# Kernel tuning notes

Hardware: AMD Instinct MI355X
Metric: run time of the kernel (lower is better)

The kernel has to match this reference:

```python
import jax, jax.numpy as jnp
import numpy as np

NUM_HEADS = 16
ROPE_BASE = 2048.0


def _rope_tables(seq_len, head_dim, dtype):
    inv_freq = 1.0 / (ROPE_BASE ** (jnp.arange(0, head_dim, 2, dtype=jnp.float32) / head_dim))
    t = jnp.arange(seq_len, dtype=jnp.float32)
    freqs = jnp.einsum('i,j->ij', t, inv_freq)          # [N, D/2]
    emb = jnp.concatenate([freqs, freqs], axis=-1)       # [N, D]
    return jnp.cos(emb).astype(dtype), jnp.sin(emb).astype(dtype)


def _rotate_half(x):
    x1, x2 = jnp.split(x, 2, axis=-1)
    return jnp.concatenate([-x2, x1], axis=-1)


def setup_inputs() -> dict:
    key = jax.random.key(0)
    k1, k2, k3, k4 = jax.random.split(key, 4)
    B, N, C = 2, 2048, 1024
    x = jax.random.normal(k1, (B, N, C), dtype=jnp.float32)
    w_qkv = jax.random.normal(k2, (3 * C, C), dtype=jnp.float32) * (C ** -0.5)
    w_proj = jax.random.normal(k3, (C, C), dtype=jnp.float32) * (C ** -0.5)
    b_proj = jnp.zeros((C,), dtype=jnp.float32)
    key_padding_mask = jax.random.randint(k4, (B, N), 0, 2, dtype=jnp.int32)
    return {"x": x, "w_qkv": w_qkv, "w_proj": w_proj, "b_proj": b_proj,
            "key_padding_mask": key_padding_mask}


def reference(x, w_qkv, w_proj, b_proj, key_padding_mask):
    B, N, C = x.shape
    H = NUM_HEADS
    D = C // H
    scale = D ** -0.5

    qkv = x @ w_qkv.T                                    # [B, N, 3C]
    q, k, v = jnp.split(qkv, 3, axis=-1)
    # [B, N, C] -> [B, H, N, D]
    q = q.reshape(B, N, H, D).transpose(0, 2, 1, 3)
    k = k.reshape(B, N, H, D).transpose(0, 2, 1, 3)
    v = v.reshape(B, N, H, D).transpose(0, 2, 1, 3)

    cos, sin = _rope_tables(N, D, x.dtype)               # [N, D]
    q = q * cos + _rotate_half(q) * sin
    k = k * cos + _rotate_half(k) * sin

    attn = jnp.einsum('bhqd,bhkd->bhqk', q, k) * scale   # [B, H, N, N]
    mask = (key_padding_mask == 0)[:, None, None, :]     # [B, 1, 1, N]
    attn = jnp.where(mask, jnp.asarray(-1e9, attn.dtype), attn)
    attn = jax.nn.softmax(attn, axis=-1)

    out = jnp.einsum('bhqk,bhkd->bhqd', attn, v)         # [B, H, N, D]
    out = out.transpose(0, 2, 1, 3).reshape(B, N, C)
    return out @ w_proj.T + b_proj
```

## Files before the change

### kernel.cpp

```cpp
#include <hip/hip_runtime.h>


typedef __attribute__((ext_vector_type(8))) short          s16x8;
typedef __attribute__((ext_vector_type(8))) unsigned short u16x8;
typedef __attribute__((ext_vector_type(4))) unsigned short u16x4;
typedef __attribute__((ext_vector_type(4))) float          f32x4;
typedef __attribute__((ext_vector_type(16))) float         f32x16;
typedef __attribute__((ext_vector_type(4))) unsigned int   u32x4;

#define MFMA_BF16(a, b, c) __builtin_amdgcn_mfma_f32_16x16x32_bf16((a), (b), (c), 0, 0, 0)
#define MFMA32_BF16(a, b, c) __builtin_amdgcn_mfma_f32_32x32x16_bf16((a), (b), (c), 0, 0, 0)

#define GLD_TO_LDS(gp, lp) __builtin_amdgcn_global_load_lds(                  \
    (const __attribute__((address_space(1))) void*)(gp),                      \
    (__attribute__((address_space(3))) void*)(lp), 16, 0, 0)

__device__ __forceinline__ unsigned short f2bf(float f) {
    union { float f; unsigned int u; } v; v.f = f;
    unsigned int u = v.u;
    unsigned int r = u + 0x7FFFu + ((u >> 16) & 1u);
    return (unsigned short)(r >> 16);
}
__device__ __forceinline__ float bf2f(unsigned short h) {
    union { unsigned int u; float f; } v; v.u = ((unsigned int)h) << 16;
    return v.f;
}
__device__ __forceinline__ f32x16 zero16() {
    f32x16 z;
#pragma unroll
    for (int i = 0; i < 16; i++) z[i] = 0.f;
    return z;
}
__device__ __forceinline__ unsigned int pkbf(float a, float b) {
    return __builtin_amdgcn_perm(__builtin_bit_cast(unsigned int, b),
                                 __builtin_bit_cast(unsigned int, a), 0x07060302u);
}
__device__ __forceinline__ int perm16(int p) {
    return (p & 3) + 8 * ((p >> 2) & 1) + 4 * (p >> 3);
}

__global__ __launch_bounds__(256) void prep(const float* __restrict__ x,
                                            const float* __restrict__ wqkv,
                                            const float* __restrict__ wproj,
                                            const int* __restrict__ m,
                                            unsigned short* __restrict__ xb,
                                            unsigned short* __restrict__ wqkvb,
                                            unsigned short* __restrict__ wprojb,
                                            unsigned short* __restrict__ mb) {
    int blk = blockIdx.x, tid = threadIdx.x;
    if (blk < 8192) {
        const float* src; unsigned short* dst; int i;
        if (blk < 4096)      { src = x;     dst = xb;     i = blk * 256 + tid; }
        else if (blk < 7168) { src = wqkv;  dst = wqkvb;  i = (blk - 4096) * 256 + tid; }
        else                 { src = wproj; dst = wprojb; i = (blk - 7168) * 256 + tid; }
        f32x4 v = ((const f32x4*)src)[i];
        u16x4 o;
        o[0] = f2bf(v[0]); o[1] = f2bf(v[1]); o[2] = f2bf(v[2]); o[3] = f2bf(v[3]);
        ((u16x4*)dst)[i] = o;
    } else {
        int i = (blk - 8192) * 256 + tid;
        int src = (i & ~15) | perm16(i & 15);
        mb[i] = (m[src] == 0) ? (unsigned short)0 : (unsigned short)0x3F80;
    }
}

__global__ __launch_bounds__(256) void gemm_bt(const unsigned short* __restrict__ A,
                                               const unsigned short* __restrict__ B,
                                               unsigned short* __restrict__ C,
                                               int M, int N, int K) {
    __shared__ unsigned short Al[128][64];
    __shared__ unsigned short Bl[128][64];
    const int tid  = threadIdx.x;
    const int lane = tid & 63;
    const int qd   = lane >> 4;
    const int cc   = lane & 15;
    const int wave = tid >> 6;
    const int wr   = wave >> 1, wc = wave & 1;
    const int nbx  = N >> 7;
    const int nwg  = gridDim.x;
    int d = blockIdx.x;
    int s = (nwg % 8 == 0) ? (d % 8) * (nwg / 8) + d / 8 : d;
    const int m0   = (s / nbx) * 128, n0 = (s % nbx) * 128;
    unsigned short* Alf = &Al[0][0];
    unsigned short* Blf = &Bl[0][0];

    f32x4 acc[4][4];
#pragma unroll
    for (int i = 0; i < 4; i++)
#pragma unroll
        for (int j = 0; j < 4; j++) acc[i][j] = (f32x4){0.f, 0.f, 0.f, 0.f};

    for (int k0 = 0; k0 < K; k0 += 64) {
#pragma unroll
        for (int t = 0; t < 4; t++) {
            int idx = t * 256 + tid;
            int row = idx >> 3, sg = (idx & 7) ^ (row & 7);
            GLD_TO_LDS(A + (size_t)(m0 + row) * K + k0 + sg * 8, Alf + idx * 8);
            GLD_TO_LDS(B + (size_t)(n0 + row) * K + k0 + sg * 8, Blf + idx * 8);
        }
        __syncthreads();
#pragma unroll
        for (int ks = 0; ks < 64; ks += 32) {
            const int s4 = ks >> 3;
            s16x8 af[4], bf[4];
#pragma unroll
            for (int i = 0; i < 4; i++) {
                int r = wr * 64 + i * 16 + cc;
                af[i] = *(const s16x8*)&Al[r][((s4 + qd) ^ (r & 7)) * 8];
            }
#pragma unroll
            for (int j = 0; j < 4; j++) {
                int r = wc * 64 + j * 16 + cc;
                bf[j] = *(const s16x8*)&Bl[r][((s4 + qd) ^ (r & 7)) * 8];
            }
#pragma unroll
            for (int i = 0; i < 4; i++)
#pragma unroll
                for (int j = 0; j < 4; j++)
                    acc[i][j] = MFMA_BF16(af[i], bf[j], acc[i][j]);
        }
        __syncthreads();
    }
#pragma unroll
    for (int i = 0; i < 4; i++)
#pragma unroll
        for (int j = 0; j < 4; j++)
#pragma unroll
            for (int r = 0; r < 4; r++) {
                int row = m0 + wr * 64 + i * 16 + qd * 4 + r;
                int col = n0 + wc * 64 + j * 16 + cc;
                C[(size_t)row * N + col] = f2bf(acc[i][j][r]);
            }
}

__global__ __launch_bounds__(256) void rope_scatter(const unsigned short* __restrict__ qkv,
                                                    const int* __restrict__ msk,
                                                    unsigned short* __restrict__ Q,
                                                    unsigned short* __restrict__ Kg,
                                                    unsigned short* __restrict__ Vt) {
    const int N = 2048, H = 16, D = 64, C3 = 3072;
    const float SCL = 0.18033688f;
    __shared__ unsigned short vl[64][65];
    const int nt = blockIdx.x, h = blockIdx.y, b = blockIdx.z;
    const int n0 = nt * 64;
    const int tid = threadIdx.x;
    const size_t bh = (size_t)b * H + h;
#pragma unroll
    for (int it = 0; it < 2; it++) {
        int idx = tid + it * 256;
        int row = idx >> 3, seg = idx & 7;
        int d0 = seg * 8;
        int n = n0 + row;
        size_t rb = ((size_t)b * N + n) * C3;
        int keep = msk[(size_t)b * N + n];
        u16x8 qv = *(const u16x8*)&qkv[rb + h * 64 + d0];
        u16x8 qp = *(const u16x8*)&qkv[rb + h * 64 + (d0 ^ 32)];
        u16x8 kv = *(const u16x8*)&qkv[rb + 1024 + h * 64 + d0];
        u16x8 kp = *(const u16x8*)&qkv[rb + 1024 + h * 64 + (d0 ^ 32)];
        u16x8 vv = *(const u16x8*)&qkv[rb + 2048 + h * 64 + d0];
        u16x8 qo, ko;
        float sgn = (d0 < 32) ? -1.0f : 1.0f;
#pragma unroll
        for (int j = 0; j < 8; j++) {
            int jj = (d0 & 31) + j;
            float th = (float)n * exp2f(-0.34375f * (float)jj);
            float cth = cosf(th), sth = sinf(th);
            qo[j] = f2bf((bf2f(qv[j]) * cth + sgn * bf2f(qp[j]) * sth) * SCL);
            ko[j] = f2bf(bf2f(kv[j]) * cth + sgn * bf2f(kp[j]) * sth);
            vl[row][d0 + j] = keep ? vv[j] : (unsigned short)0;
        }
        *(u16x8*)&Q[(bh * N + n) * D + d0]  = qo;
        *(u16x8*)&Kg[(bh * N + n) * D + d0] = ko;
    }
    __syncthreads();
#pragma unroll
    for (int it = 0; it < 2; it++) {
        int idx = tid + it * 256;
        int drow = idx >> 3, nseg = idx & 7;
        u16x8 ov;
#pragma unroll
        for (int j = 0; j < 8; j++) {
            int cpos = nseg * 8 + j;
            int srcl = (cpos & ~15) | perm16(cpos & 15);
            ov[j] = vl[srcl][drow];
        }
        *(u16x8*)&Vt[(bh * D + drow) * N + n0 + nseg * 8] = ov;
    }
}

__global__ __launch_bounds__(256, 2) void flash_attn(const unsigned short* __restrict__ Q,
                                                     const unsigned short* __restrict__ Kg,
                                                     const unsigned short* __restrict__ Vt,
                                                     const unsigned short* __restrict__ mb,
                                                     unsigned short* __restrict__ Og) {
    const int N = 2048, H = 16, D = 64;
    __shared__ unsigned short Kl0[64][64], Kl1[64][64];
    __shared__ unsigned short Vl0[64][64], Vl1[64][64];
    const int tid  = threadIdx.x;
    const int lane = tid & 63;
    const int wave = tid >> 6;
    const int c    = lane & 31;
    const int hi   = lane >> 5;
    int dd = blockIdx.x;
    int sw = (dd & 7) * 64 + (dd >> 3);
    const int qt = sw & 15, h = (sw >> 4) & 15, b = sw >> 8;
    const int q0 = qt * 128;
    const size_t bh = (size_t)b * H + h;

    s16x8 qf[4];
    {
        const unsigned short* Qb = Q + (bh * N + q0 + wave * 32 + c) * D;
#pragma unroll
        for (int kd = 0; kd < 4; kd++) qf[kd] = *(const s16x8*)(Qb + kd * 16 + hi * 8);
    }

    f32x16 o[2], lacc;
    o[0] = zero16(); o[1] = zero16(); lacc = zero16();

    const unsigned short* Kbase = Kg + bh * N * D;
    const unsigned short* Vbase = Vt + bh * D * N;
    const unsigned short* mbase = mb + (size_t)b * N;
    const int row_s = tid >> 3, sg_s = (tid & 7) ^ ((tid >> 3) & 7);
    const int row_s2 = (tid + 256) >> 3, sg_s2 = (tid & 7) ^ (((tid + 256) >> 3) & 7);

    auto issue = [&](int k0, unsigned short* Kb, unsigned short* Vb) {
        GLD_TO_LDS(Kbase + (size_t)(k0 + row_s) * D + sg_s * 8,   Kb + tid * 8);
        GLD_TO_LDS(Vbase + (size_t)row_s * N + k0 + sg_s * 8,     Vb + tid * 8);
        GLD_TO_LDS(Kbase + (size_t)(k0 + row_s2) * D + sg_s2 * 8, Kb + (tid + 256) * 8);
        GLD_TO_LDS(Vbase + (size_t)row_s2 * N + k0 + sg_s2 * 8,   Vb + (tid + 256) * 8);
    };

    auto compute = [&](int k0, const unsigned short (*Kb)[64], const unsigned short (*Vb)[64]) {
        f32x16 sst[2];
        __builtin_amdgcn_s_setprio(1);
#pragma unroll
        for (int kg = 0; kg < 2; kg++) {
            int kr = kg * 32 + c;
            f32x16 s = zero16();
#pragma unroll
            for (int kd = 0; kd < 4; kd++) {
                s16x8 kf = *(const s16x8*)&Kb[kr][((kd * 2 + hi) ^ (kr & 7)) * 8];
                s = MFMA32_BF16(kf, qf[kd], s);
            }
            sst[kg] = s;
        }
        __builtin_amdgcn_s_setprio(0);

        auto packkg = [&](int kg, s16x8* pa) {
            float p[16];
#pragma unroll
            for (int r = 0; r < 16; r++) p[r] = __builtin_amdgcn_exp2f(sst[kg][r]);
#pragma unroll
            for (int half = 0; half < 2; half++) {
                int bs = half * 8;
                u32x4 w = { pkbf(p[bs + 0], p[bs + 1]), pkbf(p[bs + 2], p[bs + 3]),
                            pkbf(p[bs + 4], p[bs + 5]), pkbf(p[bs + 6], p[bs + 7]) };
                pa[half] = __builtin_bit_cast(s16x8, w);
            }
        };

        auto pvks = [&](int ks, s16x8 pf) {
            s16x8 mfr = *(const s16x8*)&mbase[k0 + ks * 16 + hi * 8];
            __builtin_amdgcn_s_setprio(1);
            lacc = MFMA32_BF16(pf, mfr, lacc);
#pragma unroll
            for (int db = 0; db < 2; db++) {
                int vr = db * 32 + c;
                s16x8 vf = *(const s16x8*)&Vb[vr][((ks * 2 + hi) ^ (vr & 7)) * 8];
                o[db] = MFMA32_BF16(pf, vf, o[db]);
            }
            __builtin_amdgcn_s_setprio(0);
        };

        s16x8 pa[2];
        packkg(0, pa);
        pvks(0, pa[0]);
        pvks(1, pa[1]);
        packkg(1, pa);
        pvks(2, pa[0]);
        pvks(3, pa[1]);
    };

    issue(0, &Kl0[0][0], &Vl0[0][0]);
    __syncthreads();
    for (int it = 0; it < 32; it += 2) {
        int k0 = it * 64;
        if (it + 1 < 32) issue(k0 + 64, &Kl1[0][0], &Vl1[0][0]);
        compute(k0, Kl0, Vl0);
        __syncthreads();
        if (it + 2 < 32) issue(k0 + 128, &Kl0[0][0], &Vl0[0][0]);
        compute(k0 + 64, Kl1, Vl1);
        __syncthreads();
    }

    float linv[16];
#pragma unroll
    for (int r = 0; r < 16; r++) linv[r] = 1.0f / lacc[r];
#pragma unroll
    for (int db = 0; db < 2; db++)
#pragma unroll
        for (int r = 0; r < 16; r++) {
            int n = q0 + wave * 32 + (r & 3) + 8 * (r >> 2) + 4 * hi;
            Og[((size_t)b * N + n) * 1024 + h * 64 + db * 32 + c] =
                f2bf(o[db][r] * linv[r]);
        }
}

__global__ __launch_bounds__(256) void gemm_proj(const unsigned short* __restrict__ A,
                                                 const unsigned short* __restrict__ B,
                                                 float* __restrict__ C,
                                                 const float* __restrict__ bias) {
    const int NN = 1024, K = 1024;
    __shared__ unsigned short Al[128][64];
    __shared__ unsigned short Bl[64][64];
    const int tid  = threadIdx.x;
    const int lane = tid & 63;
    const int qd   = lane >> 4;
    const int cc   = lane & 15;
    const int wave = tid >> 6;
    const int wr   = wave >> 1, wc = wave & 1;
    int dd = blockIdx.x;
    int sw = (dd & 7) * 64 + (dd >> 3);
    const int m0   = (sw >> 4) * 128, n0 = (sw & 15) * 64;
    unsigned short* Alf = &Al[0][0];
    unsigned short* Blf = &Bl[0][0];

    f32x4 acc[4][2];
#pragma unroll
    for (int i = 0; i < 4; i++)
#pragma unroll
        for (int j = 0; j < 2; j++) acc[i][j] = (f32x4){0.f, 0.f, 0.f, 0.f};

    for (int k0 = 0; k0 < K; k0 += 64) {
#pragma unroll
        for (int t = 0; t < 4; t++) {
            int idx = t * 256 + tid;
            int row = idx >> 3, sg = (idx & 7) ^ (row & 7);
            GLD_TO_LDS(A + (size_t)(m0 + row) * K + k0 + sg * 8, Alf + idx * 8);
        }
#pragma unroll
        for (int t = 0; t < 2; t++) {
            int idx = t * 256 + tid;
            int row = idx >> 3, sg = (idx & 7) ^ (row & 7);
            GLD_TO_LDS(B + (size_t)(n0 + row) * K + k0 + sg * 8, Blf + idx * 8);
        }
        __syncthreads();
#pragma unroll
        for (int ks = 0; ks < 64; ks += 32) {
            const int s4 = ks >> 3;
            s16x8 af[4], bf[2];
#pragma unroll
            for (int i = 0; i < 4; i++) {
                int r = wr * 64 + i * 16 + cc;
                af[i] = *(const s16x8*)&Al[r][((s4 + qd) ^ (r & 7)) * 8];
            }
#pragma unroll
            for (int j = 0; j < 2; j++) {
                int r = wc * 32 + j * 16 + cc;
                bf[j] = *(const s16x8*)&Bl[r][((s4 + qd) ^ (r & 7)) * 8];
            }
#pragma unroll
            for (int i = 0; i < 4; i++)
#pragma unroll
                for (int j = 0; j < 2; j++)
                    acc[i][j] = MFMA_BF16(af[i], bf[j], acc[i][j]);
        }
        __syncthreads();
    }
#pragma unroll
    for (int i = 0; i < 4; i++)
#pragma unroll
        for (int j = 0; j < 2; j++)
#pragma unroll
            for (int r = 0; r < 4; r++) {
                int row = m0 + wr * 64 + i * 16 + qd * 4 + r;
                int col = n0 + wc * 32 + j * 16 + cc;
                C[(size_t)row * NN + col] = acc[i][j][r] + bias[col];
            }
}

extern "C" void kernel_launch(void* const* d_in, const int* in_sizes, int n_in,
                              void* d_out, int out_size, void* d_ws, size_t ws_size,
                              hipStream_t stream) {
    const float* x      = (const float*)d_in[0];
    const float* w_qkv  = (const float*)d_in[1];
    const float* w_proj = (const float*)d_in[2];
    const float* b_proj = (const float*)d_in[3];
    const int*   mask   = (const int*)d_in[4];
    float* out = (float*)d_out;

    unsigned short* ws     = (unsigned short*)d_ws;
    unsigned short* xb     = ws;
    unsigned short* wqkvb  = xb     + (size_t)4096 * 1024;
    unsigned short* wprojb = wqkvb  + (size_t)3072 * 1024;
    unsigned short* qkv    = wprojb + (size_t)1024 * 1024;
    unsigned short* Qm     = qkv    + (size_t)4096 * 3072;
    unsigned short* Km     = Qm     + (size_t)32 * 2048 * 64;
    unsigned short* Vtm    = Km     + (size_t)32 * 2048 * 64;
    unsigned short* attno  = Vtm    + (size_t)32 * 2048 * 64;
    unsigned short* maskbf = attno  + (size_t)4096 * 1024;

    prep<<<8208, 256, 0, stream>>>(x, w_qkv, w_proj, mask, xb, wqkvb, wprojb, maskbf);
    gemm_bt<<<768, 256, 0, stream>>>(xb, wqkvb, qkv, 4096, 3072, 1024);
    rope_scatter<<<dim3(32, 16, 2), 256, 0, stream>>>(qkv, mask, Qm, Km, Vtm);
    flash_attn<<<512, 256, 0, stream>>>(Qm, Km, Vtm, maskbf, attno);
    gemm_proj<<<512, 256, 0, stream>>>(attno, wprojb, out, b_proj);
}
```

Before: 185.8 us.

## Load K/V fragments directly from global into registers, dropping LDS staging

The flash attention kernel stops staging K and V tiles in shared memory through global_load_lds double buffering. Each wave now loads its K, V and mask fragments straight from global memory into registers, double-buffering K in registers, and all __syncthreads barriers are removed. This removes LDS traffic and block-wide synchronisation. In exchange, the four waves in a block each fetch the same K/V data separately, relying on the cache, and register pressure rises, which may lower occupancy.

```diff
diff --git a/kernel.cpp b/kernel.cpp
--- a/kernel.cpp
+++ b/kernel.cpp
@@ -194,8 +194,6 @@
                                                      const unsigned short* __restrict__ mb,
                                                      unsigned short* __restrict__ Og) {
     const int N = 2048, H = 16, D = 64;
-    __shared__ unsigned short Kl0[64][64], Kl1[64][64];
-    __shared__ unsigned short Vl0[64][64], Vl1[64][64];
     const int tid  = threadIdx.x;
     const int lane = tid & 63;
     const int wave = tid >> 6;
@@ -217,31 +215,36 @@
     f32x16 o[2], lacc;
     o[0] = zero16(); o[1] = zero16(); lacc = zero16();
 
-    const unsigned short* Kbase = Kg + bh * N * D;
-    const unsigned short* Vbase = Vt + bh * D * N;
+    const unsigned short* Krow = Kg + (bh * N + c) * D + hi * 8;
+    const unsigned short* Vrow0 = Vt + (bh * D + c) * N + hi * 8;
+    const unsigned short* Vrow1 = Vrow0 + (size_t)32 * N;
     const unsigned short* mbase = mb + (size_t)b * N;
-    const int row_s = tid >> 3, sg_s = (tid & 7) ^ ((tid >> 3) & 7);
-    const int row_s2 = (tid + 256) >> 3, sg_s2 = (tid & 7) ^ (((tid + 256) >> 3) & 7);
-
-    auto issue = [&](int k0, unsigned short* Kb, unsigned short* Vb) {
-        GLD_TO_LDS(Kbase + (size_t)(k0 + row_s) * D + sg_s * 8,   Kb + tid * 8);
-        GLD_TO_LDS(Vbase + (size_t)row_s * N + k0 + sg_s * 8,     Vb + tid * 8);
-        GLD_TO_LDS(Kbase + (size_t)(k0 + row_s2) * D + sg_s2 * 8, Kb + (tid + 256) * 8);
-        GLD_TO_LDS(Vbase + (size_t)row_s2 * N + k0 + sg_s2 * 8,   Vb + (tid + 256) * 8);
+
+    auto loadK = [&](int k0, s16x8* kf) {
+#pragma unroll
+        for (int kg = 0; kg < 2; kg++)
+#pragma unroll
+            for (int kd = 0; kd < 4; kd++)
+                kf[kg * 4 + kd] = *(const s16x8*)(Krow + (size_t)(k0 + kg * 32) * D + kd * 16);
     };
 
-    auto compute = [&](int k0, const unsigned short (*Kb)[64], const unsigned short (*Vb)[64]) {
+    auto compute = [&](int k0, const s16x8* kf) {
+        s16x8 vf[8];
+        s16x8 mfr[4];
+#pragma unroll
+        for (int ks = 0; ks < 4; ks++) {
+            vf[ks * 2 + 0] = *(const s16x8*)(Vrow0 + k0 + ks * 16);
+            vf[ks * 2 + 1] = *(const s16x8*)(Vrow1 + k0 + ks * 16);
+            mfr[ks] = *(const s16x8*)&mbase[k0 + ks * 16 + hi * 8];
+        }
+
         f32x16 sst[2];
         __builtin_amdgcn_s_setprio(1);
 #pragma unroll
         for (int kg = 0; kg < 2; kg++) {
-            int kr = kg * 32 + c;
             f32x16 s = zero16();
 #pragma unroll
-            for (int kd = 0; kd < 4; kd++) {
-                s16x8 kf = *(const s16x8*)&Kb[kr][((kd * 2 + hi) ^ (kr & 7)) * 8];
-                s = MFMA32_BF16(kf, qf[kd], s);
-            }
+            for (int kd = 0; kd < 4; kd++) s = MFMA32_BF16(kf[kg * 4 + kd], qf[kd], s);
             sst[kg] = s;
         }
         __builtin_amdgcn_s_setprio(0);
@@ -260,15 +263,10 @@
         };
 
         auto pvks = [&](int ks, s16x8 pf) {
-            s16x8 mfr = *(const s16x8*)&mbase[k0 + ks * 16 + hi * 8];
             __builtin_amdgcn_s_setprio(1);
-            lacc = MFMA32_BF16(pf, mfr, lacc);
-#pragma unroll
-            for (int db = 0; db < 2; db++) {
-                int vr = db * 32 + c;
-                s16x8 vf = *(const s16x8*)&Vb[vr][((ks * 2 + hi) ^ (vr & 7)) * 8];
-                o[db] = MFMA32_BF16(pf, vf, o[db]);
-            }
+            lacc = MFMA32_BF16(pf, mfr[ks], lacc);
+            o[0] = MFMA32_BF16(pf, vf[ks * 2 + 0], o[0]);
+            o[1] = MFMA32_BF16(pf, vf[ks * 2 + 1], o[1]);
             __builtin_amdgcn_s_setprio(0);
         };
 
@@ -281,16 +279,13 @@
         pvks(3, pa[1]);
     };
 
-    issue(0, &Kl0[0][0], &Vl0[0][0]);
-    __syncthreads();
+    s16x8 ka[8], kb[8];
+    loadK(0, ka);
     for (int it = 0; it < 32; it += 2) {
-        int k0 = it * 64;
-        if (it + 1 < 32) issue(k0 + 64, &Kl1[0][0], &Vl1[0][0]);
-        compute(k0, Kl0, Vl0);
-        __syncthreads();
-        if (it + 2 < 32) issue(k0 + 128, &Kl0[0][0], &Vl0[0][0]);
-        compute(k0 + 64, Kl1, Vl1);
-        __syncthreads();
+        loadK((it + 1) * 64, kb);
+        compute(it * 64, ka);
+        if (it + 2 < 32) loadK((it + 2) * 64, ka);
+        compute((it + 1) * 64, kb);
     }
 
     float linv[16];
```

New measurement: 260.7 us. 40.4% more time.

## Double query rows per wave in flash attention to reuse K/V fragments

Applied to the files above, without the earlier changes.

Each wave in the flash attention kernel now handles two 32-row query sub-tiles (256 queries per block instead of 128). K and V fragments read from LDS are reused across both sub-tiles, which halves LDS traffic per MFMA and halves total K/V global loads. The grid drops from 512 to 256 blocks and launch bounds go to one block per SM. That leaves only one block per CU on a 256-CU part and raises register pressure, so occupancy and latency hiding drop.

```diff
diff --git a/kernel.cpp b/kernel.cpp
--- a/kernel.cpp
+++ b/kernel.cpp
@@ -188,7 +188,7 @@
     }
 }
 
-__global__ __launch_bounds__(256, 2) void flash_attn(const unsigned short* __restrict__ Q,
+__global__ __launch_bounds__(256, 1) void flash_attn(const unsigned short* __restrict__ Q,
                                                      const unsigned short* __restrict__ Kg,
                                                      const unsigned short* __restrict__ Vt,
                                                      const unsigned short* __restrict__ mb,
@@ -202,20 +202,24 @@
     const int c    = lane & 31;
     const int hi   = lane >> 5;
     int dd = blockIdx.x;
-    int sw = (dd & 7) * 64 + (dd >> 3);
-    const int qt = sw & 15, h = (sw >> 4) & 15, b = sw >> 8;
-    const int q0 = qt * 128;
+    int sw = (dd & 7) * 32 + (dd >> 3);
+    const int qt = sw & 7, h = (sw >> 3) & 15, b = sw >> 7;
+    const int q0 = qt * 256;
     const size_t bh = (size_t)b * H + h;
 
-    s16x8 qf[4];
-    {
-        const unsigned short* Qb = Q + (bh * N + q0 + wave * 32 + c) * D;
-#pragma unroll
-        for (int kd = 0; kd < 4; kd++) qf[kd] = *(const s16x8*)(Qb + kd * 16 + hi * 8);
-    }
-
-    f32x16 o[2], lacc;
-    o[0] = zero16(); o[1] = zero16(); lacc = zero16();
+    s16x8 qf[2][4];
+#pragma unroll
+    for (int qs = 0; qs < 2; qs++) {
+        const unsigned short* Qb = Q + (bh * N + q0 + wave * 64 + qs * 32 + c) * D;
+#pragma unroll
+        for (int kd = 0; kd < 4; kd++) qf[qs][kd] = *(const s16x8*)(Qb + kd * 16 + hi * 8);
+    }
+
+    f32x16 o[2][2], lacc[2];
+#pragma unroll
+    for (int qs = 0; qs < 2; qs++) {
+        o[qs][0] = zero16(); o[qs][1] = zero16(); lacc[qs] = zero16();
+    }
 
     const unsigned short* Kbase = Kg + bh * N * D;
     const unsigned short* Vbase = Vt + bh * D * N;
@@ -231,25 +235,10 @@
     };
 
     auto compute = [&](int k0, const unsigned short (*Kb)[64], const unsigned short (*Vb)[64]) {
-        f32x16 sst[2];
-        __builtin_amdgcn_s_setprio(1);
-#pragma unroll
-        for (int kg = 0; kg < 2; kg++) {
-            int kr = kg * 32 + c;
-            f32x16 s = zero16();
-#pragma unroll
-            for (int kd = 0; kd < 4; kd++) {
-                s16x8 kf = *(const s16x8*)&Kb[kr][((kd * 2 + hi) ^ (kr & 7)) * 8];
-                s = MFMA32_BF16(kf, qf[kd], s);
-            }
-            sst[kg] = s;
-        }
-        __builtin_amdgcn_s_setprio(0);
-
-        auto packkg = [&](int kg, s16x8* pa) {
+        auto packkg = [&](const f32x16& sstv, s16x8* pa) {
             float p[16];
 #pragma unroll
-            for (int r = 0; r < 16; r++) p[r] = __builtin_amdgcn_exp2f(sst[kg][r]);
+            for (int r = 0; r < 16; r++) p[r] = __builtin_amdgcn_exp2f(sstv[r]);
 #pragma unroll
             for (int half = 0; half < 2; half++) {
                 int bs = half * 8;
@@ -259,26 +248,41 @@
             }
         };
 
-        auto pvks = [&](int ks, s16x8 pf) {
+        s16x8 pa[2][4];
+#pragma unroll
+        for (int kg = 0; kg < 2; kg++) {
+            int kr = kg * 32 + c;
+            s16x8 kf[4];
+#pragma unroll
+            for (int kd = 0; kd < 4; kd++)
+                kf[kd] = *(const s16x8*)&Kb[kr][((kd * 2 + hi) ^ (kr & 7)) * 8];
+            f32x16 sst0 = zero16(), sst1 = zero16();
+            __builtin_amdgcn_s_setprio(1);
+#pragma unroll
+            for (int kd = 0; kd < 4; kd++) {
+                sst0 = MFMA32_BF16(kf[kd], qf[0][kd], sst0);
+                sst1 = MFMA32_BF16(kf[kd], qf[1][kd], sst1);
+            }
+            __builtin_amdgcn_s_setprio(0);
+            packkg(sst0, &pa[0][kg * 2]);
+            packkg(sst1, &pa[1][kg * 2]);
+        }
+
+#pragma unroll
+        for (int ks = 0; ks < 4; ks++) {
             s16x8 mfr = *(const s16x8*)&mbase[k0 + ks * 16 + hi * 8];
+            int vr0 = c, vr1 = 32 + c;
+            s16x8 vf0 = *(const s16x8*)&Vb[vr0][((ks * 2 + hi) ^ (vr0 & 7)) * 8];
+            s16x8 vf1 = *(const s16x8*)&Vb[vr1][((ks * 2 + hi) ^ (vr1 & 7)) * 8];
             __builtin_amdgcn_s_setprio(1);
-            lacc = MFMA32_BF16(pf, mfr, lacc);
-#pragma unroll
-            for (int db = 0; db < 2; db++) {
-                int vr = db * 32 + c;
-                s16x8 vf = *(const s16x8*)&Vb[vr][((ks * 2 + hi) ^ (vr & 7)) * 8];
-                o[db] = MFMA32_BF16(pf, vf, o[db]);
+#pragma unroll
+            for (int qs = 0; qs < 2; qs++) {
+                lacc[qs] = MFMA32_BF16(pa[qs][ks], mfr, lacc[qs]);
+                o[qs][0] = MFMA32_BF16(pa[qs][ks], vf0, o[qs][0]);
+                o[qs][1] = MFMA32_BF16(pa[qs][ks], vf1, o[qs][1]);
             }
             __builtin_amdgcn_s_setprio(0);
-        };
-
-        s16x8 pa[2];
-        packkg(0, pa);
-        pvks(0, pa[0]);
-        pvks(1, pa[1]);
-        packkg(1, pa);
-        pvks(2, pa[0]);
-        pvks(3, pa[1]);
+        }
     };
 
     issue(0, &Kl0[0][0], &Vl0[0][0]);
@@ -293,17 +297,20 @@
         __syncthreads();
     }
 
-    float linv[16];
-#pragma unroll
-    for (int r = 0; r < 16; r++) linv[r] = 1.0f / lacc[r];
-#pragma unroll
-    for (int db = 0; db < 2; db++)
-#pragma unroll
-        for (int r = 0; r < 16; r++) {
-            int n = q0 + wave * 32 + (r & 3) + 8 * (r >> 2) + 4 * hi;
-            Og[((size_t)b * N + n) * 1024 + h * 64 + db * 32 + c] =
-                f2bf(o[db][r] * linv[r]);
-        }
+#pragma unroll
+    for (int qs = 0; qs < 2; qs++) {
+        float linv[16];
+#pragma unroll
+        for (int r = 0; r < 16; r++) linv[r] = 1.0f / lacc[qs][r];
+#pragma unroll
+        for (int db = 0; db < 2; db++)
+#pragma unroll
+            for (int r = 0; r < 16; r++) {
+                int n = q0 + wave * 64 + qs * 32 + (r & 3) + 8 * (r >> 2) + 4 * hi;
+                Og[((size_t)b * N + n) * 1024 + h * 64 + db * 32 + c] =
+                    f2bf(o[qs][db][r] * linv[r]);
+            }
+    }
 }
 
 __global__ __launch_bounds__(256) void gemm_proj(const unsigned short* __restrict__ A,
@@ -403,6 +410,6 @@
     prep<<<8208, 256, 0, stream>>>(x, w_qkv, w_proj, mask, xb, wqkvb, wprojb, maskbf);
     gemm_bt<<<768, 256, 0, stream>>>(xb, wqkvb, qkv, 4096, 3072, 1024);
     rope_scatter<<<dim3(32, 16, 2), 256, 0, stream>>>(qkv, mask, Qm, Km, Vtm);
-    flash_attn<<<512, 256, 0, stream>>>(Qm, Km, Vtm, maskbf, attno);
+    flash_attn<<<256, 256, 0, stream>>>(Qm, Km, Vtm, maskbf, attno);
     gemm_proj<<<512, 256, 0, stream>>>(attno, wprojb, out, b_proj);
 }
```

Result: no change. 187.7 us (+1.1%).
